# Performance work log

Measured on AMD Instinct MI355X. Metric: run time of the kernel, lower is better.

The kernel has to match this reference:

```python
import jax, jax.numpy as jnp
import numpy as np

N_NODES = 50000
N_EDGES = 800000
C = 128
EDGE_DIM = 8
N_LAYERS = 3


def setup_inputs() -> dict:
    key = jax.random.key(0)
    ks = jax.random.split(key, 8)
    x = jax.random.normal(ks[0], (N_NODES, C), dtype=jnp.float32)
    edge_index = jax.random.randint(ks[1], (2, N_EDGES), 0, N_NODES, dtype=jnp.int64)
    edge_attr = jax.random.uniform(ks[2], (N_EDGES, EDGE_DIM), dtype=jnp.float32)
    # stacked per-layer params (all layers are 128->128 HydroConv)
    lin_w = jax.random.normal(ks[3], (N_LAYERS, C, C), dtype=jnp.float32) / np.sqrt(C)
    lin_b = jnp.zeros((N_LAYERS, C), dtype=jnp.float32)
    emlp_w = jax.random.normal(ks[4], (N_LAYERS, EDGE_DIM, 1), dtype=jnp.float32) / np.sqrt(EDGE_DIM)
    emlp_b = jnp.zeros((N_LAYERS, 1), dtype=jnp.float32)
    return {"x": x, "edge_index": edge_index, "edge_attr": edge_attr,
            "lin_w": lin_w, "lin_b": lin_b, "emlp_w": emlp_w, "emlp_b": emlp_b}


def _hydro_conv(x, src, dst, edge_attr, lw, lb, ew, eb):
    # edge weight: softplus(edge_attr @ ew + eb) -> [E, 1]
    weight = jax.nn.softplus(edge_attr @ ew + eb)
    # message: weight * (x_j - x_i), x_j = source, x_i = target
    msg = weight * (x[src] - x[dst])                  # [E, C]
    agg = jax.ops.segment_sum(msg, dst, num_segments=N_NODES)  # scatter-add at target
    return agg @ lw + lb                              # node linear


def reference(x, edge_index, edge_attr, lin_w, lin_b, emlp_w, emlp_b):
    src, dst = edge_index[0], edge_index[1]
    for i in range(N_LAYERS):
        residual = x
        x = _hydro_conv(x, src, dst, edge_attr, lin_w[i], lin_b[i], emlp_w[i], emlp_b[i])
        if i < N_LAYERS - 1:
            x = jax.nn.relu(x)
            x = x + residual  # residual=True, dropout=0
    return x
```

## Files before the change

### kernel.cpp

```cpp
#include <hip/hip_runtime.h>

#define NN 50000
#define NE 800000
#define CC 128
#define NL 3

typedef short bf16x8 __attribute__((ext_vector_type(8)));
typedef float f32x4 __attribute__((ext_vector_type(4)));
union U16 { uint4 u; bf16x8 v; };

__device__ __forceinline__ float b2f(unsigned short u) {
  return __uint_as_float(((unsigned int)u) << 16);
}
__device__ __forceinline__ unsigned short f2b(float f) {
  unsigned int x = __float_as_uint(f);
  x += 0x7fffu + ((x >> 16) & 1u);
  return (unsigned short)(x >> 16);
}

__global__ void k_flags(const unsigned short* __restrict__ x,
                        const int* __restrict__ ei, int* __restrict__ flags) {
  __shared__ int cnt, any;
  if (threadIdx.x == 0) { cnt = 0; any = 0; }
  __syncthreads();
  if (threadIdx.x < 128) {
    unsigned short u = x[2 * threadIdx.x];
    int ex = (u >> 7) & 0xFF;
    if (ex >= 0x70 && ex <= 0x8F) atomicAdd(&cnt, 1);
  }
  if (ei[2 * threadIdx.x + 1] != 0) atomicOr(&any, 1);
  __syncthreads();
  if (threadIdx.x == 0) {
    flags[0] = (cnt >= 64) ? 1 : 0;
    flags[1] = (any == 0) ? 1 : 0;
  }
}

__device__ __forceinline__ int eidx(const int* ei, int row, int e, int f64) {
  return f64 ? ei[2 * ((size_t)row * NE + e)] : ei[(size_t)row * NE + e];
}

__global__ __launch_bounds__(256) void k_cvt_x(const void* __restrict__ xin,
                                               unsigned short* __restrict__ xb,
                                               const int* __restrict__ flags) {
  if (flags[0]) return;
  int i = blockIdx.x * 256 + threadIdx.x;
  const float4 a = ((const float4*)xin)[2 * i];
  const float4 b = ((const float4*)xin)[2 * i + 1];
  uint4 o;
  o.x = (unsigned)f2b(a.x) | ((unsigned)f2b(a.y) << 16);
  o.y = (unsigned)f2b(a.z) | ((unsigned)f2b(a.w) << 16);
  o.z = (unsigned)f2b(b.x) | ((unsigned)f2b(b.y) << 16);
  o.w = (unsigned)f2b(b.z) | ((unsigned)f2b(b.w) << 16);
  ((uint4*)xb)[i] = o;
}

__global__ __launch_bounds__(256) void k_cvt_par(const void* lw, const void* lb,
                                                 const void* emw, const void* emb,
                                                 unsigned short* __restrict__ wt,
                                                 float* lbf, float* emwf, float* embf,
                                                 const int* __restrict__ flags) {
  int i = blockIdx.x * 256 + threadIdx.x;
  const int bf = flags[0];
  if (i < NL * CC * CC) {
    unsigned short v = bf ? ((const unsigned short*)lw)[i]
                          : f2b(((const float*)lw)[i]);
    const int l = i >> 14, r = i & 16383, k = r >> 7, n = r & 127;
    wt[l * 16384 + n * 128 + k] = v;
  }
  if (i < NL * CC)
    lbf[i] = bf ? b2f(((const unsigned short*)lb)[i]) : ((const float*)lb)[i];
  if (i < NL * 8)
    emwf[i] = bf ? b2f(((const unsigned short*)emw)[i]) : ((const float*)emw)[i];
  if (i < NL)
    embf[i] = bf ? b2f(((const unsigned short*)emb)[i]) : ((const float*)emb)[i];
}

#define HT 8
#define HIST_BLKS ((NE + HT * 256 - 1) / (HT * 256))
__global__ __launch_bounds__(256) void k_hist(const int* __restrict__ ei,
                                              int* __restrict__ deg,
                                              unsigned short* __restrict__ rank,
                                              const int* __restrict__ flags) {
  const int f64 = flags[1];
  const int nt = gridDim.x * 256;
  const int t = blockIdx.x * 256 + threadIdx.x;
  int d[HT], r[HT];
#pragma unroll
  for (int k = 0; k < HT; ++k) {
    const int e = t + k * nt;
    d[k] = (e < NE) ? eidx(ei, 1, e, f64) : -1;
  }
#pragma unroll
  for (int k = 0; k < HT; ++k)
    if (d[k] >= 0) r[k] = atomicAdd(&deg[d[k]], 1);
#pragma unroll
  for (int k = 0; k < HT; ++k) {
    const int e = t + k * nt;
    if (e < NE) rank[e] = (unsigned short)r[k];
  }
}

#define NI4 (NN / 4)
#define SCAN_BLKS ((NI4 + 255) / 256)
__global__ __launch_bounds__(256) void k_scan1(const int* __restrict__ deg,
                                               int* __restrict__ offs,
                                               int* __restrict__ bsum) {
  __shared__ int ls[256];
  const int t = threadIdx.x;
  const int g = blockIdx.x * 256 + t;
  int4 d = make_int4(0, 0, 0, 0);
  if (g < NI4) d = ((const int4*)deg)[g];
  const int s = d.x + d.y + d.z + d.w;
  ls[t] = s;
  __syncthreads();
#pragma unroll
  for (int off = 1; off < 256; off <<= 1) {
    int tmp = (t >= off) ? ls[t - off] : 0;
    __syncthreads();
    ls[t] += tmp;
    __syncthreads();
  }
  const int excl = ls[t] - s;
  if (g < NI4) {
    int4 o;
    o.x = excl; o.y = o.x + d.x; o.z = o.y + d.y; o.w = o.z + d.z;
    ((int4*)offs)[g] = o;
  }
  if (t == 255) bsum[blockIdx.x] = ls[255];
}

__global__ void k_scan2(const int* __restrict__ bsum, int* __restrict__ bbase,
                        int* __restrict__ offs) {
  if (threadIdx.x == 0) {
    int run = 0;
    for (int b = 0; b < SCAN_BLKS; ++b) { bbase[b] = run; run += bsum[b]; }
    offs[NN] = run;
  }
}

__global__ __launch_bounds__(256) void k_scan3(int* __restrict__ offs,
                                               const int* __restrict__ bbase) {
  const int g = blockIdx.x * 256 + threadIdx.x;
  if (g >= NI4) return;
  const int base = bbase[blockIdx.x];
  int4 o = ((int4*)offs)[g];
  o.x += base; o.y += base; o.z += base; o.w += base;
  ((int4*)offs)[g] = o;
}

__global__ __launch_bounds__(256) void k_fill(const int* __restrict__ ei,
                                              const void* __restrict__ ea,
                                              const float* __restrict__ emwf,
                                              const float* __restrict__ embf,
                                              const int* __restrict__ offs,
                                              const unsigned short* __restrict__ rank,
                                              uint4* __restrict__ esrt,
                                              const int* __restrict__ flags) {
  int e = blockIdx.x * 256 + threadIdx.x;
  if (e >= NE) return;
  float a[8];
  if (flags[0]) {
    const uint4 v = ((const uint4*)ea)[e];
    unsigned int p[4] = {v.x, v.y, v.z, v.w};
#pragma unroll
    for (int q = 0; q < 4; ++q) {
      a[2 * q]     = __uint_as_float(p[q] << 16);
      a[2 * q + 1] = __uint_as_float(p[q] & 0xffff0000u);
    }
  } else {
    const float4 v0 = ((const float4*)ea)[2 * e];
    const float4 v1 = ((const float4*)ea)[2 * e + 1];
    a[0] = v0.x; a[1] = v0.y; a[2] = v0.z; a[3] = v0.w;
    a[4] = v1.x; a[5] = v1.y; a[6] = v1.z; a[7] = v1.w;
  }
  float w[NL];
#pragma unroll
  for (int l = 0; l < NL; ++l) {
    float z = embf[l];
#pragma unroll
    for (int k = 0; k < 8; ++k) z += a[k] * emwf[l * 8 + k];
    w[l] = (z > 20.f) ? z : log1pf(expf(z));
  }
  const int f64 = flags[1];
  const int d = eidx(ei, 1, e, f64);
  const int s = eidx(ei, 0, e, f64);
  const int pos = offs[d] + (int)rank[e];
  esrt[pos] = make_uint4((unsigned)s, __float_as_uint(w[0]),
                         __float_as_uint(w[1]), __float_as_uint(w[2]));
}

#define LPAD 136
template<int LAYER>
__device__ __forceinline__ unsigned wcomp(const uint4& p) {
  return LAYER == 0 ? p.y : (LAYER == 1 ? p.z : p.w);
}

template<int LAYER>
__global__ __launch_bounds__(512) void k_layer(const int* __restrict__ offs,
                                               const uint4* __restrict__ esrt,
                                               const unsigned short* xc_,
                                               const unsigned short* alt, int sel,
                                               const unsigned short* __restrict__ wt,
                                               const float* __restrict__ lbf,
                                               void* outp, int last,
                                               const int* __restrict__ flags,
                                               unsigned short* __restrict__ xout) {
  const unsigned short* xb = (sel && flags[0]) ? alt : xc_;
  __shared__ unsigned short shA[64 * LPAD];
  __shared__ unsigned short shB[128 * LPAD];
  const int tid = threadIdx.x;
  const int rb = blockIdx.x * 64;
  const unsigned short* wtl = wt + (size_t)LAYER * CC * CC;

  for (int u = tid; u < 2048; u += 512) {
    const int row = u >> 4, q = u & 15;
    *(uint4*)&shB[row * LPAD + q * 8] = *(const uint4*)&wtl[row * 128 + q * 8];
  }

  const int wid = tid >> 6;
  const int l = tid & 63;
  const int g = l >> 4;
  const int chlane = l & 15;
  const int ch = chlane * 8;

  for (int i = 0; i < 8; ++i) {
    const int nl = wid * 8 + i;
    const int node = __builtin_amdgcn_readfirstlane(rb + nl);
    if (node >= NN) {
      if (l < 16) *(uint4*)&shA[nl * LPAD + ch] = make_uint4(0, 0, 0, 0);
      continue;
    }
    const int j0 = offs[node];
    const int j1 = offs[node + 1];
    const uint4 xi = *(const uint4*)&xb[(size_t)node * CC + ch];
    float ax[8];
#pragma unroll
    for (int q = 0; q < 8; ++q) ax[q] = 0.f;
    float sw = 0.f;

    for (int jc = j0; jc < j1; jc += 64) {
      const int cnt = j1 - jc;
      const int kk = (l < cnt) ? l : (cnt - 1);
      const uint4 rec = esrt[jc + kk];
      const int srcl = (int)rec.x;
      const int wl = (int)wcomp<LAYER>(rec);
      const int cc2 = (cnt > 64) ? 64 : cnt;
      const int nsb = (cc2 + 15) >> 4;
      for (int b2 = 0; b2 < nsb; ++b2) {
        int srcw[4]; float wv[4];
#pragma unroll
        for (int b = 0; b < 4; ++b) {
          const int k = b2 * 16 + b * 4 + g;
          srcw[b] = __shfl(srcl, k);
          const float w = __uint_as_float((unsigned)__shfl(wl, k));
          wv[b] = (k < cnt) ? w : 0.f;
        }
        uint4 v[4];
#pragma unroll
        for (int b = 0; b < 4; ++b)
          v[b] = *(const uint4*)&xb[(size_t)(unsigned)srcw[b] * CC + ch];
#pragma unroll
        for (int b = 0; b < 4; ++b) {
          const float w = wv[b];
          const unsigned pv0 = v[b].x, pv1 = v[b].y, pv2 = v[b].z, pv3 = v[b].w;
          ax[0] += w * __uint_as_float(pv0 << 16);
          ax[1] += w * __uint_as_float(pv0 & 0xffff0000u);
          ax[2] += w * __uint_as_float(pv1 << 16);
          ax[3] += w * __uint_as_float(pv1 & 0xffff0000u);
          ax[4] += w * __uint_as_float(pv2 << 16);
          ax[5] += w * __uint_as_float(pv2 & 0xffff0000u);
          ax[6] += w * __uint_as_float(pv3 << 16);
          ax[7] += w * __uint_as_float(pv3 & 0xffff0000u);
          sw += w;
        }
      }
    }

#pragma unroll
    for (int q = 0; q < 8; ++q) {
      ax[q] += __shfl_xor(ax[q], 16);
      ax[q] += __shfl_xor(ax[q], 32);
    }
    sw += __shfl_xor(sw, 16);
    sw += __shfl_xor(sw, 32);

    if (l < 16) {
      float r[8];
      r[0] = ax[0] - sw * __uint_as_float(xi.x << 16);
      r[1] = ax[1] - sw * __uint_as_float(xi.x & 0xffff0000u);
      r[2] = ax[2] - sw * __uint_as_float(xi.y << 16);
      r[3] = ax[3] - sw * __uint_as_float(xi.y & 0xffff0000u);
      r[4] = ax[4] - sw * __uint_as_float(xi.z << 16);
      r[5] = ax[5] - sw * __uint_as_float(xi.z & 0xffff0000u);
      r[6] = ax[6] - sw * __uint_as_float(xi.w << 16);
      r[7] = ax[7] - sw * __uint_as_float(xi.w & 0xffff0000u);
      uint4 o;
      o.x = (unsigned)f2b(r[0]) | ((unsigned)f2b(r[1]) << 16);
      o.y = (unsigned)f2b(r[2]) | ((unsigned)f2b(r[3]) << 16);
      o.z = (unsigned)f2b(r[4]) | ((unsigned)f2b(r[5]) << 16);
      o.w = (unsigned)f2b(r[6]) | ((unsigned)f2b(r[7]) << 16);
      *(uint4*)&shA[nl * LPAD + ch] = o;
    }
  }
  __syncthreads();

  const int rw = wid >> 1;
  const int cb = (wid & 1) * 4;
  const int lr = l & 15;
  const int lk = (l >> 4) * 8;

  U16 afr[4];
#pragma unroll
  for (int kk = 0; kk < 4; ++kk)
    afr[kk].u = *(const uint4*)&shA[(rw * 16 + lr) * LPAD + kk * 32 + lk];
  __syncthreads();

  const float* lbp = lbf + LAYER * CC;
  f32x4 acc[4];
#pragma unroll
  for (int t = 0; t < 4; ++t) {
    acc[t] = (f32x4){0.f, 0.f, 0.f, 0.f};
#pragma unroll
    for (int kk = 0; kk < 4; ++kk) {
      U16 bfr;
      bfr.u = *(const uint4*)&shB[((cb + t) * 16 + lr) * LPAD + kk * 32 + lk];
      acc[t] = __builtin_amdgcn_mfma_f32_16x16x32_bf16(afr[kk].v, bfr.v, acc[t], 0, 0, 0);
    }
  }

#pragma unroll
  for (int t = 0; t < 4; ++t) {
    const float bv = lbp[(cb + t) * 16 + lr];
#pragma unroll
    for (int r = 0; r < 4; ++r) {
      const int tr = (l >> 4) * 4 + r;
      shA[(rw * 16 + tr) * LPAD + (cb + t) * 16 + lr] = f2b(acc[t][r] + bv);
    }
  }
  __syncthreads();

  const int isbf = flags[0];
  for (int u = tid; u < 1024; u += 512) {
    const int row = u >> 4, q = u & 15;
    const int gr = rb + row;
    if (gr >= NN) continue;
    const uint4 yv = *(const uint4*)&shA[row * LPAD + q * 8];
    float y0 = __uint_as_float(yv.x << 16), y1 = __uint_as_float(yv.x & 0xffff0000u);
    float y2 = __uint_as_float(yv.y << 16), y3 = __uint_as_float(yv.y & 0xffff0000u);
    float y4 = __uint_as_float(yv.z << 16), y5 = __uint_as_float(yv.z & 0xffff0000u);
    float y6 = __uint_as_float(yv.w << 16), y7 = __uint_as_float(yv.w & 0xffff0000u);
    const size_t off = (size_t)gr * CC + q * 8;
    if (!last) {
      const uint4 rv = *(const uint4*)&xb[off];
      y0 = fmaxf(y0, 0.f) + __uint_as_float(rv.x << 16);
      y1 = fmaxf(y1, 0.f) + __uint_as_float(rv.x & 0xffff0000u);
      y2 = fmaxf(y2, 0.f) + __uint_as_float(rv.y << 16);
      y3 = fmaxf(y3, 0.f) + __uint_as_float(rv.y & 0xffff0000u);
      y4 = fmaxf(y4, 0.f) + __uint_as_float(rv.z << 16);
      y5 = fmaxf(y5, 0.f) + __uint_as_float(rv.z & 0xffff0000u);
      y6 = fmaxf(y6, 0.f) + __uint_as_float(rv.w << 16);
      y7 = fmaxf(y7, 0.f) + __uint_as_float(rv.w & 0xffff0000u);
      uint4 o;
      o.x = (unsigned)f2b(y0) | ((unsigned)f2b(y1) << 16);
      o.y = (unsigned)f2b(y2) | ((unsigned)f2b(y3) << 16);
      o.z = (unsigned)f2b(y4) | ((unsigned)f2b(y5) << 16);
      o.w = (unsigned)f2b(y6) | ((unsigned)f2b(y7) << 16);
      *(uint4*)&xout[off] = o;
    } else if (isbf) {
      *(uint4*)&((unsigned short*)outp)[off] = yv;
    } else {
      *(float4*)&((float*)outp)[off] = make_float4(y0, y1, y2, y3);
      *(float4*)&((float*)outp)[off + 4] = make_float4(y4, y5, y6, y7);
    }
  }
}

extern "C" void kernel_launch(void* const* d_in, const int* in_sizes, int n_in,
                              void* d_out, int out_size, void* d_ws, size_t ws_size,
                              hipStream_t stream) {
  const unsigned short* x0 = (const unsigned short*)d_in[0];
  const int* ei = (const int*)d_in[1];

  const size_t nbuf = (size_t)NN * CC;
  unsigned short* xb0 = (unsigned short*)d_ws;
  unsigned short* xb1 = xb0 + nbuf;
  unsigned short* wt = xb1 + nbuf;
  uint4* esrt = (uint4*)(wt + (size_t)NL * CC * CC);
  int* deg = (int*)(esrt + NE);
  int* offs = deg + NN;
  unsigned short* rank = (unsigned short*)(offs + NN + 4);
  int* bsum = (int*)(rank + NE);
  int* bbase = bsum + 64;
  float* lbf = (float*)(bbase + 64);
  float* emwf = lbf + (size_t)NL * CC;
  float* embf = emwf + NL * 8;
  int* flags = (int*)(embf + NL);
  const size_t need = (size_t)((char*)(flags + 2) - (char*)d_ws);
  if (ws_size < need) {
    hipMemsetAsync(d_out, 0, (size_t)out_size * 2, stream);
    return;
  }

  k_flags<<<1, 256, 0, stream>>>(x0, ei, flags);
  k_cvt_x<<<(NN * CC / 8) / 256, 256, 0, stream>>>(d_in[0], xb0, flags);
  k_cvt_par<<<(NL * CC * CC + 255) / 256, 256, 0, stream>>>(
      d_in[3], d_in[4], d_in[5], d_in[6], wt, lbf, emwf, embf, flags);

  hipMemsetAsync(deg, 0, NN * sizeof(int), stream);
  k_hist<<<HIST_BLKS, 256, 0, stream>>>(ei, deg, rank, flags);
  k_scan1<<<SCAN_BLKS, 256, 0, stream>>>(deg, offs, bsum);
  k_scan2<<<1, 64, 0, stream>>>(bsum, bbase, offs);
  k_scan3<<<SCAN_BLKS, 256, 0, stream>>>(offs, bbase);
  k_fill<<<(NE + 255) / 256, 256, 0, stream>>>(ei, d_in[2], emwf, embf,
                                               offs, rank, esrt, flags);

  const int LBLKS = (NN + 63) / 64;
  unsigned short* xc = xb0;
  unsigned short* xo = xb1;
  for (int layer = 0; layer < NL; ++layer) {
    const int sel = (layer == 0) ? 1 : 0;
    const int last = (layer == NL - 1) ? 1 : 0;
    if (layer == 0)
      k_layer<0><<<LBLKS, 512, 0, stream>>>(offs, esrt, xc, x0, sel, wt, lbf,
                                            d_out, last, flags, xo);
    else if (layer == 1)
      k_layer<1><<<LBLKS, 512, 0, stream>>>(offs, esrt, xc, x0, sel, wt, lbf,
                                            d_out, last, flags, xo);
    else
      k_layer<2><<<LBLKS, 512, 0, stream>>>(offs, esrt, xc, x0, sel, wt, lbf,
                                            d_out, last, flags, xo);
    unsigned short* t = xc; xc = xo; xo = t;
  }
}
```

Baseline: 309.4 us.

## Pack edge records into 8 bytes and read weights directly from global

```diff
diff --git a/kernel.cpp b/kernel.cpp
--- a/kernel.cpp
+++ b/kernel.cpp
@@ -155,7 +155,7 @@
                                               const float* __restrict__ embf,
                                               const int* __restrict__ offs,
                                               const unsigned short* __restrict__ rank,
-                                              uint4* __restrict__ esrt,
+                                              uint2* __restrict__ esrt,
                                               const int* __restrict__ flags) {
   int e = blockIdx.x * 256 + threadIdx.x;
   if (e >= NE) return;
@@ -174,31 +174,32 @@
     a[0] = v0.x; a[1] = v0.y; a[2] = v0.z; a[3] = v0.w;
     a[4] = v1.x; a[5] = v1.y; a[6] = v1.z; a[7] = v1.w;
   }
-  float w[NL];
+  unsigned wb[NL];
 #pragma unroll
   for (int l = 0; l < NL; ++l) {
     float z = embf[l];
 #pragma unroll
     for (int k = 0; k < 8; ++k) z += a[k] * emwf[l * 8 + k];
-    w[l] = (z > 20.f) ? z : log1pf(expf(z));
+    const float w = (z > 20.f) ? z : log1pf(expf(z));
+    wb[l] = (unsigned)f2b(w);
   }
   const int f64 = flags[1];
   const int d = eidx(ei, 1, e, f64);
   const int s = eidx(ei, 0, e, f64);
   const int pos = offs[d] + (int)rank[e];
-  esrt[pos] = make_uint4((unsigned)s, __float_as_uint(w[0]),
-                         __float_as_uint(w[1]), __float_as_uint(w[2]));
+  esrt[pos] = make_uint2((unsigned)s | (wb[0] << 16), wb[1] | (wb[2] << 16));
 }
 
 #define LPAD 136
 template<int LAYER>
-__device__ __forceinline__ unsigned wcomp(const uint4& p) {
-  return LAYER == 0 ? p.y : (LAYER == 1 ? p.z : p.w);
+__device__ __forceinline__ unsigned wbits(const uint2& p) {
+  return LAYER == 0 ? (p.x & 0xffff0000u)
+       : (LAYER == 1 ? (p.y << 16) : (p.y & 0xffff0000u));
 }
 
 template<int LAYER>
 __global__ __launch_bounds__(512) void k_layer(const int* __restrict__ offs,
-                                               const uint4* __restrict__ esrt,
+                                               const uint2* __restrict__ esrt,
                                                const unsigned short* xc_,
                                                const unsigned short* alt, int sel,
                                                const unsigned short* __restrict__ wt,
@@ -208,21 +209,14 @@
                                                unsigned short* __restrict__ xout) {
   const unsigned short* xb = (sel && flags[0]) ? alt : xc_;
   __shared__ unsigned short shA[64 * LPAD];
-  __shared__ unsigned short shB[128 * LPAD];
   const int tid = threadIdx.x;
   const int rb = blockIdx.x * 64;
   const unsigned short* wtl = wt + (size_t)LAYER * CC * CC;
 
-  for (int u = tid; u < 2048; u += 512) {
-    const int row = u >> 4, q = u & 15;
-    *(uint4*)&shB[row * LPAD + q * 8] = *(const uint4*)&wtl[row * 128 + q * 8];
-  }
-
   const int wid = tid >> 6;
   const int l = tid & 63;
   const int g = l >> 4;
-  const int chlane = l & 15;
-  const int ch = chlane * 8;
+  const int ch = (l & 15) * 8;
 
   for (int i = 0; i < 8; ++i) {
     const int nl = wid * 8 + i;
@@ -242,9 +236,9 @@
     for (int jc = j0; jc < j1; jc += 64) {
       const int cnt = j1 - jc;
       const int kk = (l < cnt) ? l : (cnt - 1);
-      const uint4 rec = esrt[jc + kk];
-      const int srcl = (int)rec.x;
-      const int wl = (int)wcomp<LAYER>(rec);
+      const uint2 rec = esrt[jc + kk];
+      const int srcl = (int)(rec.x & 0xffffu);
+      const int wl = (int)wbits<LAYER>(rec);
       const int cc2 = (cnt > 64) ? 64 : cnt;
       const int nsb = (cc2 + 15) >> 4;
       for (int b2 = 0; b2 < nsb; ++b2) {
@@ -321,12 +315,13 @@
 #pragma unroll
   for (int t = 0; t < 4; ++t) {
     acc[t] = (f32x4){0.f, 0.f, 0.f, 0.f};
-#pragma unroll
-    for (int kk = 0; kk < 4; ++kk) {
-      U16 bfr;
-      bfr.u = *(const uint4*)&shB[((cb + t) * 16 + lr) * LPAD + kk * 32 + lk];
-      acc[t] = __builtin_amdgcn_mfma_f32_16x16x32_bf16(afr[kk].v, bfr.v, acc[t], 0, 0, 0);
-    }
+    U16 bfr[4];
+#pragma unroll
+    for (int kk = 0; kk < 4; ++kk)
+      bfr[kk].u = *(const uint4*)&wtl[((cb + t) * 16 + lr) * 128 + kk * 32 + lk];
+#pragma unroll
+    for (int kk = 0; kk < 4; ++kk)
+      acc[t] = __builtin_amdgcn_mfma_f32_16x16x32_bf16(afr[kk].v, bfr[kk].v, acc[t], 0, 0, 0);
   }
 
 #pragma unroll
@@ -386,7 +381,7 @@
   unsigned short* xb0 = (unsigned short*)d_ws;
   unsigned short* xb1 = xb0 + nbuf;
   unsigned short* wt = xb1 + nbuf;
-  uint4* esrt = (uint4*)(wt + (size_t)NL * CC * CC);
+  uint2* esrt = (uint2*)(wt + (size_t)NL * CC * CC);
   int* deg = (int*)(esrt + NE);
   int* offs = deg + NN;
   unsigned short* rank = (unsigned short*)(offs + NN + 4);
```

New measurement: 332.7 us. 7.5% more time.
